# Kernel optimization log

Measured on AMD Instinct MI355X. Metric: run time of the kernel, lower is better.

## Reference

```python
import jax, jax.numpy as jnp
import numpy as np

DECAY_RATE = 0.95
EPSILON = 1e-6
N_HEAD = 16


def setup_inputs() -> dict:
    key = jax.random.key(0)
    ks = jax.random.split(key, 9)
    B, L, D, H = 2, 2048, 1024, N_HEAD
    s = 1.0 / np.sqrt(D)
    return {
        "x": jax.random.normal(ks[0], (B, L, D), dtype=jnp.float32),
        "Wq": jax.random.normal(ks[1], (D, D), dtype=jnp.float32) * s,
        "Wk": jax.random.normal(ks[2], (D, D), dtype=jnp.float32) * s,
        "Wv": jax.random.normal(ks[3], (D, D), dtype=jnp.float32) * s,
        "Wo": jax.random.normal(ks[4], (D, D), dtype=jnp.float32) * s,
        "Ww": jax.random.normal(ks[5], (H, D), dtype=jnp.float32) * s,
        "bw": jnp.zeros((H,), dtype=jnp.float32),
        "We": jax.random.normal(ks[6], (H, D), dtype=jnp.float32) * s,
        "be": jnp.zeros((H,), dtype=jnp.float32),
    }


def _phi(x):
    # Non-negative feature map: elu(x) + 1
    return jax.nn.elu(x) + 1.0


def _heads(t, H):
    B, L, D = t.shape
    return t.reshape(B, L, H, D // H).transpose(0, 2, 1, 3)  # (B,H,L,dh)


def reference(x, Wq, Wk, Wv, Wo, Ww, bw, We, be):
    B, L, D = x.shape
    H = N_HEAD

    Q = _phi(_heads(x @ Wq.T, H))  # (B,H,L,dh)
    K = _phi(_heads(x @ Wk.T, H))
    V = _heads(x @ Wv.T, H)

    # per-head scalar gates, shape (B,H,L)
    write_gate = jax.nn.sigmoid(x @ Ww.T + bw).transpose(0, 2, 1)
    erase_gate = jax.nn.sigmoid(x @ We.T + be).transpose(0, 2, 1)

    # gated decay unrolled via log-space cumsum -> causal decay matrix
    g = (1.0 - erase_gate) * DECAY_RATE
    C = jnp.cumsum(jnp.log(g + 1e-8), axis=-1)        # (B,H,L)
    decay_logits = C[:, :, :, None] - C[:, :, None, :]  # (B,H,L,L)
    causal = jnp.tril(jnp.ones((L, L), dtype=bool))
    decay_matrix = jnp.exp(jnp.where(causal, decay_logits, -jnp.inf))

    scores = jnp.einsum("bhid,bhjd->bhij", Q, K)
    eff = scores * write_gate[:, :, None, :] * decay_matrix  # (B,H,L,L)

    retrieved = jnp.einsum("bhij,bhjd->bhid", eff, V)
    denom = jnp.sum(eff, axis=-1, keepdims=True)
    out = retrieved / (denom + EPSILON)                # (B,H,L,dh)

    out = out.transpose(0, 2, 1, 3).reshape(B, L, D)
    return out @ Wo.T
```

## Files before the change

### kernel.cpp

```cpp
#include <hip/hip_runtime.h>
#include <hip/hip_bf16.h>
#include <math.h>

#define B_ 2
#define L_ 2048
#define D_ 1024
#define H_ 16
#define DH 64
#define ML (B_*L_)
#define QKV_N 3072

typedef __attribute__((ext_vector_type(8)))  short bf16x8;
typedef __attribute__((ext_vector_type(4)))  float f32x4;
typedef __attribute__((ext_vector_type(16))) float f32x16;
typedef unsigned short u16;

__device__ __forceinline__ u16 f2bf(float f) {
    union { float f; unsigned u; } v; v.f = f;
    unsigned r = (v.u + 0x7FFFu + ((v.u >> 16) & 1u)) >> 16;
    return (u16)r;
}

__device__ __forceinline__ float bf2f(short s) {
    union { unsigned u; float f; } v;
    v.u = ((unsigned)(unsigned short)s) << 16;
    return v.f;
}

__device__ __forceinline__ float fexp2(float x) {
    float r; asm("v_exp_f32 %0, %1" : "=v"(r) : "v"(x)); return r;
}

__device__ __forceinline__ void async16(void* lds, const void* g) {
    __builtin_amdgcn_global_load_lds(
        (__attribute__((address_space(1))) unsigned int*)g,
        (__attribute__((address_space(3))) unsigned int*)lds,
        16, 0, 0);
}

__device__ __forceinline__ void xcd_decode(int id, int& mt, int& nt) {
    int xcd = id & 7;
    int r = id >> 3;
    nt = r >> 2;
    mt = (xcd << 2) | (r & 3);
}

__global__ __launch_bounds__(256)
void prep_kernel(const float* __restrict__ x,
                 const float* __restrict__ Wq, const float* __restrict__ Wk,
                 const float* __restrict__ Wv, const float* __restrict__ Wo,
                 const float* __restrict__ Ww, const float* __restrict__ We,
                 u16* __restrict__ Wcat, u16* __restrict__ xb,
                 u16* __restrict__ WG2) {
    int blk = blockIdx.x, t = threadIdx.x;
    if (blk < 4096) {
        int i = (blk * 256 + t) * 4;
        int sel = i >> 20;
        const float* s = sel == 0 ? Wq : sel == 1 ? Wk : sel == 2 ? Wv : Wo;
        float4 v = *(const float4*)(s + (i & 1048575));
        ushort4 o;
        o.x = f2bf(v.x); o.y = f2bf(v.y); o.z = f2bf(v.z); o.w = f2bf(v.w);
        *(ushort4*)(Wcat + i) = o;
    } else if (blk < 8192) {
        int i = ((blk - 4096) * 256 + t) * 4;
        float4 v = *(const float4*)(x + i);
        ushort4 o;
        o.x = f2bf(v.x); o.y = f2bf(v.y); o.z = f2bf(v.z); o.w = f2bf(v.w);
        *(ushort4*)(xb + i) = o;
    } else {
        int i = ((blk - 8192) * 256 + t) * 4;
        const float* s = (i < 16384) ? (Ww + i) : (We + i - 16384);
        float4 v = *(const float4*)s;
        ushort4 o;
        o.x = f2bf(v.x); o.y = f2bf(v.y); o.z = f2bf(v.z); o.w = f2bf(v.w);
        *(ushort4*)(WG2 + i) = o;
    }
}

__global__ __launch_bounds__(64)
void scan_kernel(const float* __restrict__ GLOG, const float* __restrict__ LWG,
                 float* __restrict__ CC, float* __restrict__ CJW) {
    int bh = blockIdx.x;
    int lane = threadIdx.x;
    const float* src = GLOG + (size_t)bh * L_;
    const float* lw  = LWG  + (size_t)bh * L_;
    float* dst  = CC  + (size_t)bh * L_;
    float* dstw = CJW + (size_t)bh * L_;
    float running = 0.f;
    for (int base = 0; base < L_; base += 64) {
        float v = src[base + lane];
#pragma unroll
        for (int off = 1; off < 64; off <<= 1) {
            float u = __shfl_up(v, off, 64);
            if (lane >= off) v += u;
        }
        float c = running + v;
        dst[base + lane]  = c;
        dstw[base + lane] = c - lw[base + lane];
        running += __shfl(v, 63, 64);
    }
}

__global__ __launch_bounds__(256)
void gemm_fused(const u16* __restrict__ A, const u16* __restrict__ Bw,
                u16* __restrict__ QKo, u16* __restrict__ Ktb,
                u16* __restrict__ Vtb, const u16* __restrict__ WG2,
                const float* __restrict__ bw, const float* __restrict__ be,
                float* __restrict__ GLOG, float* __restrict__ LWG,
                int K) {
    __shared__ u16 As[2][8192];
    __shared__ u16 Bs[2][8192];
    int t = threadIdx.x;
    int lane = t & 63;
    int w = t >> 6, wm = w >> 1, wn = w & 1;
    int l15 = lane & 15, l4 = lane >> 4;
    int mt, nt;
    xcd_decode((int)blockIdx.x, mt, nt);
    int m0 = mt * 128, n0 = nt * 128;
    bool gate = (nt == 24);
    const u16* Bbase = gate ? WG2 : (Bw + (size_t)n0 * K);

    f32x4 zz = {0.f, 0.f, 0.f, 0.f};
    f32x4 acc[4][4];
#pragma unroll
    for (int m = 0; m < 4; m++)
#pragma unroll
        for (int n = 0; n < 4; n++) acc[m][n] = zz;

    auto STAGE = [&](int buf, int k0) {
#pragma unroll
        for (int i = 0; i < 4; i++) {
            int c = i * 256 + t;
            int row = c >> 3;
            int ch = (c & 7) ^ (row & 7);
            async16(&As[buf][c * 8], A     + (size_t)(m0 + row) * K + k0 + ch * 8);
            async16(&Bs[buf][c * 8], Bbase + (size_t)row * K + k0 + ch * 8);
        }
    };

    STAGE(0, 0);
    __syncthreads();

    int KT = K >> 6, cur = 0;
    for (int kt = 0; kt < KT; kt++) {
        if (kt + 1 < KT) STAGE(cur ^ 1, (kt + 1) << 6);

        bf16x8 af[4][2], bfr[4][2];
#pragma unroll
        for (int ks = 0; ks < 2; ks++) {
#pragma unroll
            for (int m = 0; m < 4; m++) {
                int row = wm * 64 + m * 16 + l15;
                int ch = (l4 + 4 * ks) ^ (row & 7);
                af[m][ks] = *(const bf16x8*)&As[cur][row * 64 + ch * 8];
            }
#pragma unroll
            for (int n = 0; n < 4; n++) {
                int row = wn * 64 + n * 16 + l15;
                int ch = (l4 + 4 * ks) ^ (row & 7);
                bfr[n][ks] = *(const bf16x8*)&Bs[cur][row * 64 + ch * 8];
            }
        }
#pragma unroll
        for (int m = 0; m < 4; m++)
#pragma unroll
            for (int n = 0; n < 4; n++) {
                acc[m][n] = __builtin_amdgcn_mfma_f32_16x16x32_bf16(af[m][0], bfr[n][0], acc[m][n], 0, 0, 0);
                acc[m][n] = __builtin_amdgcn_mfma_f32_16x16x32_bf16(af[m][1], bfr[n][1], acc[m][n], 0, 0, 0);
            }

        __syncthreads();
        cur ^= 1;
    }

    if (gate) {
#pragma unroll
        for (int m = 0; m < 4; m++)
#pragma unroll
            for (int n = 0; n < 4; n++) {
                int g = wn * 64 + n * 16 + l15;
                if (g < 32) {
                    int h = g & 15;
                    int rowb = m0 + wm * 64 + m * 16 + l4 * 4;
#pragma unroll
                    for (int r = 0; r < 4; r++) {
                        int row = rowb + r;
                        size_t idx = ((size_t)((row >> 11) * 16 + h)) * 2048 + (row & 2047);
                        float val = acc[m][n][r];
                        if (g < 16) {
                            float wgv = 1.f / (1.f + __expf(-(val + bw[h])));
                            LWG[idx] = __log2f(wgv);
                        } else {
                            float egv = 1.f / (1.f + __expf(-(val + be[h])));
                            GLOG[idx] = __log2f((1.f - egv) * 0.95f + 1e-8f);
                        }
                    }
                }
            }
        return;
    }

#pragma unroll
    for (int m = 0; m < 4; m++)
#pragma unroll
        for (int n = 0; n < 4; n++) {
            int colb = n0 + wn * 64 + n * 16 + l15;
            int rowb = m0 + wm * 64 + m * 16 + l4 * 4;
            if (colb < 1024) {
#pragma unroll
                for (int r = 0; r < 4; r++) {
                    float c = acc[m][n][r];
                    c = (c > 0.f) ? (c + 1.f) : __expf(c);
                    QKo[(size_t)(rowb + r) * 2048 + colb] = f2bf(c);
                }
            } else if (colb < 2048) {
                ushort4 o;
                u16 bv[4];
#pragma unroll
                for (int r = 0; r < 4; r++) {
                    float c = acc[m][n][r];
                    c = (c > 0.f) ? (c + 1.f) : __expf(c);
                    bv[r] = f2bf(c);
                    QKo[(size_t)(rowb + r) * 2048 + colb] = bv[r];
                }
                o.x = bv[0]; o.y = bv[1]; o.z = bv[2]; o.w = bv[3];
                int kcol = colb - 1024;
                int bb = rowb >> 11;
                *(ushort4*)&Ktb[((size_t)((bb * 16 + (kcol >> 6)) * 64 + (kcol & 63))) * 2048 + (rowb & 2047)] = o;
            } else {
                int vcol = colb - 2048;
                int bb = rowb >> 11;
                ushort4 o;
                o.x = f2bf(acc[m][n][0]); o.y = f2bf(acc[m][n][1]);
                o.z = f2bf(acc[m][n][2]); o.w = f2bf(acc[m][n][3]);
                *(ushort4*)&Vtb[((size_t)((bb * 16 + (vcol >> 6)) * 64 + (vcol & 63))) * 2048 + (rowb & 2047)] = o;
            }
        }
}

__global__ __launch_bounds__(256)
void gemm_wo64(const u16* __restrict__ A, const u16* __restrict__ Bw,
               float* __restrict__ Cout, int MT, int N, int K) {
    __shared__ u16 As[2][4096];
    __shared__ u16 Bs[2][8192];
    int t = threadIdx.x;
    int id = (int)blockIdx.x;
    int lane = t & 63;
    int w = t >> 6, wm = w >> 1, wn = w & 1;
    int l15 = lane & 15, l4 = lane >> 4;
    int m0 = (id % MT) * 64, n0 = (id / MT) * 128;

    f32x4 zz = {0.f, 0.f, 0.f, 0.f};
    f32x4 acc[2][4];
#pragma unroll
    for (int m = 0; m < 2; m++)
#pragma unroll
        for (int n = 0; n < 4; n++) acc[m][n] = zz;

    auto STAGE = [&](int buf, int k0) {
#pragma unroll
        for (int i = 0; i < 2; i++) {
            int c = i * 256 + t;
            int row = c >> 3;
            int ch = (c & 7) ^ (row & 7);
            async16(&As[buf][c * 8], A + (size_t)(m0 + row) * K + k0 + ch * 8);
        }
#pragma unroll
        for (int i = 0; i < 4; i++) {
            int c = i * 256 + t;
            int row = c >> 3;
            int ch = (c & 7) ^ (row & 7);
            async16(&Bs[buf][c * 8], Bw + (size_t)(n0 + row) * K + k0 + ch * 8);
        }
    };

    STAGE(0, 0);
    __syncthreads();

    int KT = K >> 6, cur = 0;
    for (int kt = 0; kt < KT; kt++) {
        if (kt + 1 < KT) STAGE(cur ^ 1, (kt + 1) << 6);

        bf16x8 af[2][2], bfr[4][2];
#pragma unroll
        for (int ks = 0; ks < 2; ks++) {
#pragma unroll
            for (int m = 0; m < 2; m++) {
                int row = wm * 32 + m * 16 + l15;
                int ch = (l4 + 4 * ks) ^ (row & 7);
                af[m][ks] = *(const bf16x8*)&As[cur][row * 64 + ch * 8];
            }
#pragma unroll
            for (int n = 0; n < 4; n++) {
                int row = wn * 64 + n * 16 + l15;
                int ch = (l4 + 4 * ks) ^ (row & 7);
                bfr[n][ks] = *(const bf16x8*)&Bs[cur][row * 64 + ch * 8];
            }
        }
#pragma unroll
        for (int m = 0; m < 2; m++)
#pragma unroll
            for (int n = 0; n < 4; n++) {
                acc[m][n] = __builtin_amdgcn_mfma_f32_16x16x32_bf16(af[m][0], bfr[n][0], acc[m][n], 0, 0, 0);
                acc[m][n] = __builtin_amdgcn_mfma_f32_16x16x32_bf16(af[m][1], bfr[n][1], acc[m][n], 0, 0, 0);
            }

        __syncthreads();
        cur ^= 1;
    }

#pragma unroll
    for (int m = 0; m < 2; m++)
#pragma unroll
        for (int n = 0; n < 4; n++) {
            int colb = n0 + wn * 64 + n * 16 + l15;
            int rowb = m0 + wm * 32 + m * 16 + l4 * 4;
#pragma unroll
            for (int r = 0; r < 4; r++)
                Cout[(size_t)(rowb + r) * N + colb] = acc[m][n][r];
        }
}

__global__ __launch_bounds__(128)
void state_delta(const u16* __restrict__ Ktb, const u16* __restrict__ Vtb,
                 const float* __restrict__ CCg, const float* __restrict__ CJWg,
                 u16* __restrict__ dSg, float* __restrict__ dZg) {
    __shared__ u16 Kts[4096], Vts[4096];
    __shared__ float cjl[64];
    int c = blockIdx.x, bh = blockIdx.y;
    int j0 = c * 64;
    int t = threadIdx.x, w = t >> 6, lane = t & 63, l31 = lane & 31, hi = lane >> 5;
    const u16* ktg = Ktb + (size_t)(bh * 64) * 2048 + j0;
    const u16* vtg = Vtb + (size_t)(bh * 64) * 2048 + j0;
#pragma unroll
    for (int rnd = 0; rnd < 4; rnd++) {
        int cc_ = rnd * 128 + t; int row = cc_ >> 3; int ch = (cc_ & 7) ^ (row & 7);
        async16(&Kts[cc_ * 8], ktg + (size_t)row * 2048 + ch * 8);
        async16(&Vts[cc_ * 8], vtg + (size_t)row * 2048 + ch * 8);
    }
    if (t < 64) cjl[t] = CJWg[(size_t)bh * L_ + j0 + t];
    float cref = CCg[(size_t)bh * L_ + j0 + 63];
    __syncthreads();

    f32x16 zz16;
#pragma unroll
    for (int r = 0; r < 16; r++) zz16[r] = 0.f;
    int swz = l31 & 7;
    int vq = w;
    u16* base = dSg + (size_t)(bh * 32 + c) * 4096;

#pragma unroll
    for (int kq = 0; kq < 2; kq++) {
        f32x16 acc = zz16;
        float zs = 0.f;
#pragma unroll
        for (int ks = 0; ks < 4; ks++) {
            int ch = (ks * 2 + hi) ^ swz;
            bf16x8 kt = *(const bf16x8*)&Kts[(kq * 32 + l31) * 64 + ch * 8];
            bf16x8 vt = *(const bf16x8*)&Vts[(vq * 32 + l31) * 64 + ch * 8];
            union { unsigned u[4]; bf16x8 v; } kw;
#pragma unroll
            for (int e2 = 0; e2 < 4; e2++) {
                int jb = ks * 16 + hi * 8 + e2 * 2;
                float f0 = bf2f(kt[e2 * 2 + 0]) * fexp2(cref - cjl[jb]);
                float f1 = bf2f(kt[e2 * 2 + 1]) * fexp2(cref - cjl[jb + 1]);
                zs += f0 + f1;
                asm("v_cvt_pk_bf16_f32 %0, %1, %2" : "=v"(kw.u[e2]) : "v"(f0), "v"(f1));
            }
            acc = __builtin_amdgcn_mfma_f32_32x32x16_bf16(vt, kw.v, acc, 0, 0, 0);
        }
#pragma unroll
        for (int r = 0; r < 16; r++) {
            int v = vq * 32 + (r & 3) + 8 * (r >> 2) + 4 * hi;
            base[v * 64 + kq * 32 + l31] = f2bf(acc[r]);
        }
        if (w == 0) {
            zs += __shfl_xor(zs, 32, 64);
            if (hi == 0)
                dZg[(size_t)(bh * 32 + c) * 64 + kq * 32 + l31] = zs;
        }
    }
}

__global__ __launch_bounds__(256)
void state_scan(const u16* __restrict__ dSg, const float* __restrict__ dZg,
                const float* __restrict__ CCg,
                u16* __restrict__ Sg, float* __restrict__ Zg) {
    __shared__ float lam[32];
    int bh = blockIdx.x, slice = blockIdx.y;
    int t = threadIdx.x;
    if (t < 32) {
        float cr = CCg[(size_t)bh * L_ + t * 64 + 63];
        float cp = t ? CCg[(size_t)bh * L_ + t * 64 - 1] : 0.f;
        lam[t] = t ? fexp2(cr - cp) : 0.f;
    }
    __syncthreads();
    if (slice < 8) {
        int eidx = slice * 512 + t * 2;
        float s0 = 0.f, s1 = 0.f;
#pragma unroll 8
        for (int c = 0; c < 32; c++) {
            unsigned d = *(const unsigned*)&dSg[(size_t)(bh * 32 + c) * 4096 + eidx];
            float l = lam[c];
            s0 = l * s0 + bf2f((short)(d & 0xffff));
            s1 = l * s1 + bf2f((short)(d >> 16));
            unsigned o;
            asm("v_cvt_pk_bf16_f32 %0, %1, %2" : "=v"(o) : "v"(s0), "v"(s1));
            *(unsigned*)&Sg[(size_t)(bh * 32 + c) * 4096 + eidx] = o;
        }
    } else if (t < 64) {
        float z = 0.f;
#pragma unroll 8
        for (int c = 0; c < 32; c++) {
            z = lam[c] * z + dZg[(size_t)(bh * 32 + c) * 64 + t];
            Zg[(size_t)(bh * 32 + c) * 64 + t] = z;
        }
    }
}

__global__ __launch_bounds__(128)
void attn_out(const u16* __restrict__ QK, const u16* __restrict__ Vtb,
              const u16* __restrict__ Sg, const float* __restrict__ Zg,
              const float* __restrict__ CCg, const float* __restrict__ CJWg,
              u16* __restrict__ AOb) {
    __shared__ u16 Qs[4096], Ks[4096], Vts[4096], Ss[4096];
    __shared__ float ccl[64], cjl[64], zbl[64];
    int c = blockIdx.x, bh = blockIdx.y;
    int b = bh >> 4, h = bh & 15;
    int j0 = c * 64;
    int t = threadIdx.x, w = t >> 6, lane = t & 63, l31 = lane & 31, hi = lane >> 5;
    int w32 = w * 32;

    const u16* qkg = QK + (size_t)(b * L_ + j0) * 2048 + h * 64;
    const u16* vtg = Vtb + (size_t)(bh * 64) * 2048 + j0;
#pragma unroll
    for (int rnd = 0; rnd < 4; rnd++) {
        int cc_ = rnd * 128 + t; int row = cc_ >> 3; int ch = (cc_ & 7) ^ (row & 7);
        async16(&Qs[cc_ * 8],  qkg + (size_t)row * 2048 + ch * 8);
        async16(&Ks[cc_ * 8],  qkg + (size_t)row * 2048 + 1024 + ch * 8);
        async16(&Vts[cc_ * 8], vtg + (size_t)row * 2048 + ch * 8);
    }
    if (c) {
        const u16* sg = Sg + (size_t)(bh * 32 + c - 1) * 4096;
#pragma unroll
        for (int rnd = 0; rnd < 4; rnd++) {
            int cc_ = rnd * 128 + t; int row = cc_ >> 3; int ch = (cc_ & 7) ^ (row & 7);
            async16(&Ss[cc_ * 8], sg + row * 64 + ch * 8);
        }
        if (t < 64) zbl[t] = Zg[(size_t)(bh * 32 + c - 1) * 64 + t];
    }
    if (t < 64) {
        ccl[t] = CCg[(size_t)bh * L_ + j0 + t];
        cjl[t] = CJWg[(size_t)bh * L_ + j0 + t];
    }
    float cpv = c ? CCg[(size_t)bh * L_ + j0 - 1] : 0.f;
    __syncthreads();

    f32x16 zz16;
#pragma unroll
    for (int r = 0; r < 16; r++) zz16[r] = 0.f;
    int swz = l31 & 7;

    bf16x8 qb[4];
#pragma unroll
    for (int ks = 0; ks < 4; ks++) {
        int ch = (ks * 2 + hi) ^ swz;
        qb[ks] = *(const bf16x8*)&Qs[(w32 + l31) * 64 + ch * 8];
    }
    float ci = ccl[w32 + l31];

    f32x16 st[2];
    st[0] = zz16; st[1] = zz16;
    __builtin_amdgcn_s_setprio(1);
#pragma unroll
    for (int ks = 0; ks < 4; ks++) {
        int ch = (ks * 2 + hi) ^ swz;
        bf16x8 k0 = *(const bf16x8*)&Ks[l31 * 64 + ch * 8];
        bf16x8 k1 = *(const bf16x8*)&Ks[(32 + l31) * 64 + ch * 8];
        st[0] = __builtin_amdgcn_mfma_f32_32x32x16_bf16(k0, qb[ks], st[0], 0, 0, 0);
        st[1] = __builtin_amdgcn_mfma_f32_32x32x16_bf16(k1, qb[ks], st[1], 0, 0, 0);
    }
    __builtin_amdgcn_s_setprio(0);

    unsigned pk[2][4][2];
    float dloc = 0.f;
    int lim = w32 + l31;
#pragma unroll
    for (int n = 0; n < 2; n++) {
#pragma unroll
        for (int rq = 0; rq < 4; rq++) {
            float4 cj4 = *(const float4*)&cjl[n * 32 + rq * 8 + hi * 4];
            float e0 = st[n][rq * 4 + 0] * fexp2(ci - cj4.x);
            float e1 = st[n][rq * 4 + 1] * fexp2(ci - cj4.y);
            float e2 = st[n][rq * 4 + 2] * fexp2(ci - cj4.z);
            float e3 = st[n][rq * 4 + 3] * fexp2(ci - cj4.w);
            int jb = n * 32 + rq * 8 + hi * 4;
            e0 = (jb + 0 <= lim) ? e0 : 0.f;
            e1 = (jb + 1 <= lim) ? e1 : 0.f;
            e2 = (jb + 2 <= lim) ? e2 : 0.f;
            e3 = (jb + 3 <= lim) ? e3 : 0.f;
            dloc += (e0 + e1) + (e2 + e3);
            asm("v_cvt_pk_bf16_f32 %0, %1, %2" : "=v"(pk[n][rq][0]) : "v"(e0), "v"(e1));
            asm("v_cvt_pk_bf16_f32 %0, %1, %2" : "=v"(pk[n][rq][1]) : "v"(e2), "v"(e3));
        }
    }

    f32x16 acc0 = zz16, acc1 = zz16;
    __builtin_amdgcn_s_setprio(1);
#pragma unroll
    for (int wi = 0; wi < 4; wi++) {
        int n = wi >> 1, qA = 2 * (wi & 1), qB = qA + 1;
        unsigned a0 = pk[n][qA][0], b0 = pk[n][qB][0];
        unsigned a1 = pk[n][qA][1], b1 = pk[n][qB][1];
        asm volatile("v_permlane32_swap_b32 %0, %1" : "+v"(a0), "+v"(b0));
        asm volatile("v_permlane32_swap_b32 %0, %1" : "+v"(a1), "+v"(b1));
        union { unsigned u[4]; bf16x8 v; } aw;
        aw.u[0] = a0; aw.u[1] = a1; aw.u[2] = b0; aw.u[3] = b1;
        int jc = (wi * 2 + hi) ^ swz;
        bf16x8 v0 = *(const bf16x8*)&Vts[l31 * 64 + jc * 8];
        bf16x8 v1 = *(const bf16x8*)&Vts[(32 + l31) * 64 + jc * 8];
        acc0 = __builtin_amdgcn_mfma_f32_32x32x16_bf16(aw.v, v0, acc0, 0, 0, 0);
        acc1 = __builtin_amdgcn_mfma_f32_32x32x16_bf16(aw.v, v1, acc1, 0, 0, 0);
    }
    __builtin_amdgcn_s_setprio(0);

    if (c) {
        f32x16 oi0 = zz16, oi1 = zz16;
        __builtin_amdgcn_s_setprio(1);
#pragma unroll
        for (int ks = 0; ks < 4; ks++) {
            int ch = (ks * 2 + hi) ^ swz;
            bf16x8 s0 = *(const bf16x8*)&Ss[l31 * 64 + ch * 8];
            bf16x8 s1 = *(const bf16x8*)&Ss[(32 + l31) * 64 + ch * 8];
            oi0 = __builtin_amdgcn_mfma_f32_32x32x16_bf16(qb[ks], s0, oi0, 0, 0, 0);
            oi1 = __builtin_amdgcn_mfma_f32_32x32x16_bf16(qb[ks], s1, oi1, 0, 0, 0);
        }
        __builtin_amdgcn_s_setprio(0);
#pragma unroll
        for (int r = 0; r < 16; r++) {
            int il = (r & 3) + 8 * (r >> 2) + 4 * hi;
            float sc = fexp2(ccl[w32 + il] - cpv);
            acc0[r] += sc * oi0[r];
            acc1[r] += sc * oi1[r];
        }
        float dq = 0.f;
#pragma unroll
        for (int ks = 0; ks < 4; ks++)
#pragma unroll
            for (int e = 0; e < 8; e++)
                dq += bf2f(qb[ks][e]) * zbl[ks * 16 + hi * 8 + e];
        dloc += fexp2(ci - cpv) * dq;
    }

    float dl = dloc + __shfl_xor(dloc, 32, 64);
#pragma unroll
    for (int r = 0; r < 16; r++) {
        int il = (r & 3) + 8 * (r >> 2) + 4 * hi;
        float dv = __shfl(dl, il, 64);
        float inv = 1.f / (dv + 1e-6f);
        int ig = j0 + w32 + il;
        AOb[(size_t)(b * L_ + ig) * D_ + h * DH + l31]      = f2bf(acc0[r] * inv);
        AOb[(size_t)(b * L_ + ig) * D_ + h * DH + 32 + l31] = f2bf(acc1[r] * inv);
    }
}

extern "C" void kernel_launch(void* const* d_in, const int* in_sizes, int n_in,
                              void* d_out, int out_size, void* d_ws, size_t ws_size,
                              hipStream_t stream) {
    const float* x  = (const float*)d_in[0];
    const float* Wq = (const float*)d_in[1];
    const float* Wk = (const float*)d_in[2];
    const float* Wv = (const float*)d_in[3];
    const float* Wo = (const float*)d_in[4];
    const float* Ww = (const float*)d_in[5];
    const float* bw = (const float*)d_in[6];
    const float* We = (const float*)d_in[7];
    const float* be = (const float*)d_in[8];
    float* out = (float*)d_out;

    char* wsb = (char*)d_ws;
    u16* xb   = (u16*)(wsb);
    u16* Sg   = xb;
    u16* Wcat = (u16*)(wsb + ((size_t)8  << 20));
    u16* QK   = (u16*)(wsb + ((size_t)16 << 20));
    u16* Vtb  = (u16*)(wsb + ((size_t)32 << 20));
    u16* Ktb  = (u16*)(wsb + ((size_t)40 << 20));
    u16* AOb  = (u16*)(wsb + ((size_t)48 << 20));
    u16* dSg  = AOb;
    float* GLOG = (float*)(wsb + ((size_t)56 << 20));
    float* LWG  = GLOG + 65536;
    float* CC   = LWG  + 65536;
    float* CJW  = CC   + 65536;
    float* dZg  = CJW  + 65536;
    float* Zg   = dZg  + 65536;
    u16*  WG2  = (u16*)(Zg + 65536);

    prep_kernel<<<8224, 256, 0, stream>>>(
        x, Wq, Wk, Wv, Wo, Ww, We, Wcat, xb, WG2);

    gemm_fused<<<32 * 25, 256, 0, stream>>>(
        xb, Wcat, QK, Ktb, Vtb, WG2, bw, be, GLOG, LWG, D_);

    scan_kernel<<<B_ * H_, 64, 0, stream>>>(GLOG, LWG, CC, CJW);

    state_delta<<<dim3(32, B_ * H_), 128, 0, stream>>>(Ktb, Vtb, CC, CJW, dSg, dZg);
    state_scan<<<dim3(B_ * H_, 9), 256, 0, stream>>>(dSg, dZg, CC, Sg, Zg);
    attn_out<<<dim3(32, B_ * H_), 128, 0, stream>>>(QK, Vtb, Sg, Zg, CC, CJW, AOb);

    gemm_wo64<<<(ML / 64) * (D_ / 128), 256, 0, stream>>>(
        AOb, Wcat + (size_t)3072 * 1024, out, ML / 64, D_, D_);
}
```

Baseline: 108.4 us.

## Eliminate global scan kernel by computing chunk-local cumulative log-decay inside consumers

Removes the separate serial scan_kernel that produced global cumulative log-decay arrays. Each consumer kernel now computes a chunk-local prefix sum with wave shuffles, and state_scan derives the inter-chunk decay factors from per-chunk sums. Since only differences of cumulative sums are used, chunk-relative values stay equivalent. This saves a launch and a serial, low-parallelism pass, at the cost of redundant shuffle work in each block.

```diff
diff --git a/kernel.cpp b/kernel.cpp
--- a/kernel.cpp
+++ b/kernel.cpp
@@ -77,30 +77,6 @@
     }
 }
 
-__global__ __launch_bounds__(64)
-void scan_kernel(const float* __restrict__ GLOG, const float* __restrict__ LWG,
-                 float* __restrict__ CC, float* __restrict__ CJW) {
-    int bh = blockIdx.x;
-    int lane = threadIdx.x;
-    const float* src = GLOG + (size_t)bh * L_;
-    const float* lw  = LWG  + (size_t)bh * L_;
-    float* dst  = CC  + (size_t)bh * L_;
-    float* dstw = CJW + (size_t)bh * L_;
-    float running = 0.f;
-    for (int base = 0; base < L_; base += 64) {
-        float v = src[base + lane];
-#pragma unroll
-        for (int off = 1; off < 64; off <<= 1) {
-            float u = __shfl_up(v, off, 64);
-            if (lane >= off) v += u;
-        }
-        float c = running + v;
-        dst[base + lane]  = c;
-        dstw[base + lane] = c - lw[base + lane];
-        running += __shfl(v, 63, 64);
-    }
-}
-
 __global__ __launch_bounds__(256)
 void gemm_fused(const u16* __restrict__ A, const u16* __restrict__ Bw,
                 u16* __restrict__ QKo, u16* __restrict__ Ktb,
@@ -323,10 +299,11 @@
 
 __global__ __launch_bounds__(128)
 void state_delta(const u16* __restrict__ Ktb, const u16* __restrict__ Vtb,
-                 const float* __restrict__ CCg, const float* __restrict__ CJWg,
+                 const float* __restrict__ GLOG, const float* __restrict__ LWG,
                  u16* __restrict__ dSg, float* __restrict__ dZg) {
     __shared__ u16 Kts[4096], Vts[4096];
     __shared__ float cjl[64];
+    __shared__ float creff;
     int c = blockIdx.x, bh = blockIdx.y;
     int j0 = c * 64;
     int t = threadIdx.x, w = t >> 6, lane = t & 63, l31 = lane & 31, hi = lane >> 5;
@@ -338,9 +315,19 @@
         async16(&Kts[cc_ * 8], ktg + (size_t)row * 2048 + ch * 8);
         async16(&Vts[cc_ * 8], vtg + (size_t)row * 2048 + ch * 8);
     }
-    if (t < 64) cjl[t] = CJWg[(size_t)bh * L_ + j0 + t];
-    float cref = CCg[(size_t)bh * L_ + j0 + 63];
+    if (t < 64) {
+        float v = GLOG[(size_t)bh * L_ + j0 + t];
+        float lw = LWG[(size_t)bh * L_ + j0 + t];
+#pragma unroll
+        for (int off = 1; off < 64; off <<= 1) {
+            float u = __shfl_up(v, off, 64);
+            if (t >= off) v += u;
+        }
+        cjl[t] = v - lw;
+        if (t == 63) creff = v;
+    }
     __syncthreads();
+    float cref = creff;
 
     f32x16 zz16;
 #pragma unroll
@@ -384,15 +371,21 @@
 
 __global__ __launch_bounds__(256)
 void state_scan(const u16* __restrict__ dSg, const float* __restrict__ dZg,
-                const float* __restrict__ CCg,
+                const float* __restrict__ GLOG,
                 u16* __restrict__ Sg, float* __restrict__ Zg) {
     __shared__ float lam[32];
     int bh = blockIdx.x, slice = blockIdx.y;
     int t = threadIdx.x;
-    if (t < 32) {
-        float cr = CCg[(size_t)bh * L_ + t * 64 + 63];
-        float cp = t ? CCg[(size_t)bh * L_ + t * 64 - 1] : 0.f;
-        lam[t] = t ? fexp2(cr - cp) : 0.f;
+    {
+        int cc8 = t >> 3, p8 = t & 7;
+        const float* gl = GLOG + (size_t)bh * L_ + cc8 * 64 + p8 * 8;
+        float s = 0.f;
+#pragma unroll
+        for (int e = 0; e < 8; e++) s += gl[e];
+        s += __shfl_xor(s, 1, 64);
+        s += __shfl_xor(s, 2, 64);
+        s += __shfl_xor(s, 4, 64);
+        if (p8 == 0) lam[cc8] = cc8 ? fexp2(s) : 0.f;
     }
     __syncthreads();
     if (slice < 8) {
@@ -421,7 +414,7 @@
 __global__ __launch_bounds__(128)
 void attn_out(const u16* __restrict__ QK, const u16* __restrict__ Vtb,
               const u16* __restrict__ Sg, const float* __restrict__ Zg,
-              const float* __restrict__ CCg, const float* __restrict__ CJWg,
+              const float* __restrict__ GLOG, const float* __restrict__ LWG,
               u16* __restrict__ AOb) {
     __shared__ u16 Qs[4096], Ks[4096], Vts[4096], Ss[4096];
     __shared__ float ccl[64], cjl[64], zbl[64];
@@ -450,10 +443,16 @@
         if (t < 64) zbl[t] = Zg[(size_t)(bh * 32 + c - 1) * 64 + t];
     }
     if (t < 64) {
-        ccl[t] = CCg[(size_t)bh * L_ + j0 + t];
-        cjl[t] = CJWg[(size_t)bh * L_ + j0 + t];
-    }
-    float cpv = c ? CCg[(size_t)bh * L_ + j0 - 1] : 0.f;
+        float v = GLOG[(size_t)bh * L_ + j0 + t];
+        float lw = LWG[(size_t)bh * L_ + j0 + t];
+#pragma unroll
+        for (int off = 1; off < 64; off <<= 1) {
+            float u = __shfl_up(v, off, 64);
+            if (t >= off) v += u;
+        }
+        ccl[t] = v;
+        cjl[t] = v - lw;
+    }
     __syncthreads();
 
     f32x16 zz16;
@@ -539,7 +538,7 @@
 #pragma unroll
         for (int r = 0; r < 16; r++) {
             int il = (r & 3) + 8 * (r >> 2) + 4 * hi;
-            float sc = fexp2(ccl[w32 + il] - cpv);
+            float sc = fexp2(ccl[w32 + il]);
             acc0[r] += sc * oi0[r];
             acc1[r] += sc * oi1[r];
         }
@@ -549,7 +548,7 @@
 #pragma unroll
             for (int e = 0; e < 8; e++)
                 dq += bf2f(qb[ks][e]) * zbl[ks * 16 + hi * 8 + e];
-        dloc += fexp2(ci - cpv) * dq;
+        dloc += fexp2(ci) * dq;
     }
 
     float dl = dloc + __shfl_xor(dloc, 32, 64);
@@ -589,9 +588,7 @@
     u16* dSg  = AOb;
     float* GLOG = (float*)(wsb + ((size_t)56 << 20));
     float* LWG  = GLOG + 65536;
-    float* CC   = LWG  + 65536;
-    float* CJW  = CC   + 65536;
-    float* dZg  = CJW  + 65536;
+    float* dZg  = LWG  + 65536;
     float* Zg   = dZg  + 65536;
     u16*  WG2  = (u16*)(Zg + 65536);
 
@@ -601,11 +598,9 @@
     gemm_fused<<<32 * 25, 256, 0, stream>>>(
         xb, Wcat, QK, Ktb, Vtb, WG2, bw, be, GLOG, LWG, D_);
 
-    scan_kernel<<<B_ * H_, 64, 0, stream>>>(GLOG, LWG, CC, CJW);
-
-    state_delta<<<dim3(32, B_ * H_), 128, 0, stream>>>(Ktb, Vtb, CC, CJW, dSg, dZg);
-    state_scan<<<dim3(B_ * H_, 9), 256, 0, stream>>>(dSg, dZg, CC, Sg, Zg);
-    attn_out<<<dim3(32, B_ * H_), 128, 0, stream>>>(QK, Vtb, Sg, Zg, CC, CJW, AOb);
+    state_delta<<<dim3(32, B_ * H_), 128, 0, stream>>>(Ktb, Vtb, GLOG, LWG, dSg, dZg);
+    state_scan<<<dim3(B_ * H_, 9), 256, 0, stream>>>(dSg, dZg, GLOG, Sg, Zg);
+    attn_out<<<dim3(32, B_ * H_), 128, 0, stream>>>(QK, Vtb, Sg, Zg, GLOG, LWG, AOb);
 
     gemm_wo64<<<(ML / 64) * (D_ / 128), 256, 0, stream>>>(
         AOb, Wcat + (size_t)3072 * 1024, out, ML / 64, D_, D_);
```

Measured after the change: 98.90 us (median of 2 runs). 1.1x faster.
